# Kernel tuning notes

Hardware: AMD Instinct MI355X
Metric: run time of the kernel (lower is better)

## Reference

```python
import jax, jax.numpy as jnp
import numpy as np

B, TQ, TB, C, H, INNER = 4, 4096, 2048, 512, 8, 2048
D = C // H


def _ln(x, g, b, eps=1e-5):
    m = x.mean(-1, keepdims=True)
    v = ((x - m) ** 2).mean(-1, keepdims=True)
    return (x - m) / jnp.sqrt(v + eps) * g + b


def _heads(t):
    b, t_, _ = t.shape
    return t.reshape(b, t_, H, D).transpose(0, 2, 1, 3)  # (B,h,T,d)


def _merge(t):
    b, _, t_, _ = t.shape
    return t.transpose(0, 2, 1, 3).reshape(b, t_, C)


def _lin(x, w, b):
    return x @ w + b


def _forward(x, y0, y1,
             ln1_g, ln1_b, ln2_0_g, ln2_0_b, ln2_1_g, ln2_1_b,
             ln3_g, ln3_b, ln4_g, ln4_b, ln5_g, ln5_b,
             ca_q_w, ca_q_b, ca_k0_w, ca_k0_b, ca_v0_w, ca_v0_b,
             ca_k1_w, ca_k1_b, ca_v1_w, ca_v1_b, ca_p_w, ca_p_b,
             sa_q_w, sa_q_b, sa_k_w, sa_k_b, sa_v_w, sa_v_b, sa_p_w, sa_p_b,
             m1_w1, m1_b1, m1_w2, m1_b2, m2_w1, m2_b1, m2_w2, m2_b2):
    # ---- cross-attention (LinearCrossAttention, accumulate over branches) ----
    xn = _ln(x, ln1_g, ln1_b)
    q = jax.nn.softmax(_heads(_lin(xn, ca_q_w, ca_q_b)), axis=-1)  # (B,h,TQ,d)
    out = q
    branches = [(y0, ln2_0_g, ln2_0_b, ca_k0_w, ca_k0_b, ca_v0_w, ca_v0_b),
                (y1, ln2_1_g, ln2_1_b, ca_k1_w, ca_k1_b, ca_v1_w, ca_v1_b)]
    for yi, g, bb, kw, kb, vw, vb in branches:
        yn = _ln(yi, g, bb)
        k = jax.nn.softmax(_heads(_lin(yn, kw, kb)), axis=-1)  # (B,h,TB,d)
        v = _heads(_lin(yn, vw, vb))
        k_sum = k.sum(axis=-2, keepdims=True)                   # (B,h,1,d)
        d_inv = 1.0 / jnp.clip((q * k_sum).sum(-1, keepdims=True), 1e-9)
        ctx = jnp.einsum('bhtd,bhte->bhde', k, v)               # (B,h,d,d)
        out = out + (q @ ctx) * d_inv
    x = x + _lin(_merge(out), ca_p_w, ca_p_b)

    # ---- MLP 1 ----
    h1 = _lin(_ln(x, ln3_g, ln3_b), m1_w1, m1_b1)
    x = x + _lin(jax.nn.gelu(h1, approximate=False), m1_w2, m1_b2)

    # ---- self-attention (LinearAttention, attn_type='l1') ----
    xn = _ln(x, ln4_g, ln4_b)
    q = jax.nn.softmax(_heads(_lin(xn, sa_q_w, sa_q_b)), axis=-1)
    k = jax.nn.softmax(_heads(_lin(xn, sa_k_w, sa_k_b)), axis=-1)
    v = _heads(_lin(xn, sa_v_w, sa_v_b))
    k_sum = k.sum(axis=-2, keepdims=True)
    d_inv = 1.0 / (q * k_sum).sum(-1, keepdims=True)
    ctx = jnp.einsum('bhtd,bhte->bhde', k, v)
    sa = (q @ ctx) * d_inv + q
    x = x + _lin(_merge(sa), sa_p_w, sa_p_b)

    # ---- MLP 2 ----
    h2 = _lin(_ln(x, ln5_g, ln5_b), m2_w1, m2_b1)
    x = x + _lin(jax.nn.gelu(h2, approximate=False), m2_w2, m2_b2)
    return x


def setup_inputs() -> dict:
    key = jax.random.key(0)
    ks = iter(jax.random.split(key, 64))
    s = 1.0 / np.sqrt(C)
    si = 1.0 / np.sqrt(INNER)

    def lin_p(din, dout, scale):
        return (jax.random.normal(next(ks), (din, dout), jnp.float32) * scale,
                jnp.zeros((dout,), jnp.float32))

    inp = {
        'x': jax.random.normal(next(ks), (B, TQ, C), jnp.float32),
        'y0': jax.random.normal(next(ks), (B, TB, C), jnp.float32),
        'y1': jax.random.normal(next(ks), (B, TB, C), jnp.float32),
    }
    for nm in ['ln1', 'ln2_0', 'ln2_1', 'ln3', 'ln4', 'ln5']:
        inp[nm + '_g'] = jnp.ones((C,), jnp.float32)
        inp[nm + '_b'] = jnp.zeros((C,), jnp.float32)
    for nm in ['ca_q', 'ca_k0', 'ca_v0', 'ca_k1', 'ca_v1', 'ca_p',
               'sa_q', 'sa_k', 'sa_v', 'sa_p']:
        w, b = lin_p(C, C, s)
        inp[nm + '_w'] = w
        inp[nm + '_b'] = b
    for nm in ['m1', 'm2']:
        w1, b1 = lin_p(C, INNER, s)
        w2, b2 = lin_p(INNER, C, si)
        inp[nm + '_w1'], inp[nm + '_b1'] = w1, b1
        inp[nm + '_w2'], inp[nm + '_b2'] = w2, b2
    return inp


def reference(x, y0, y1,
              ln1_g, ln1_b, ln2_0_g, ln2_0_b, ln2_1_g, ln2_1_b,
              ln3_g, ln3_b, ln4_g, ln4_b, ln5_g, ln5_b,
              ca_q_w, ca_q_b, ca_k0_w, ca_k0_b, ca_v0_w, ca_v0_b,
              ca_k1_w, ca_k1_b, ca_v1_w, ca_v1_b, ca_p_w, ca_p_b,
              sa_q_w, sa_q_b, sa_k_w, sa_k_b, sa_v_w, sa_v_b, sa_p_w, sa_p_b,
              m1_w1, m1_b1, m1_w2, m1_b2, m2_w1, m2_b1, m2_w2, m2_b2):
    return _forward(x, y0, y1,
                    ln1_g, ln1_b, ln2_0_g, ln2_0_b, ln2_1_g, ln2_1_b,
                    ln3_g, ln3_b, ln4_g, ln4_b, ln5_g, ln5_b,
                    ca_q_w, ca_q_b, ca_k0_w, ca_k0_b, ca_v0_w, ca_v0_b,
                    ca_k1_w, ca_k1_b, ca_v1_w, ca_v1_b, ca_p_w, ca_p_b,
                    sa_q_w, sa_q_b, sa_k_w, sa_k_b, sa_v_w, sa_v_b, sa_p_w, sa_p_b,
                    m1_w1, m1_b1, m1_w2, m1_b2, m2_w1, m2_b1, m2_w2, m2_b2)
```

## Files before the change

### kernel.cpp

```cpp
#include <hip/hip_runtime.h>
#include <hip/hip_bf16.h>
#include <math.h>

#define NBATCH 4
#define TQD 4096
#define TBD 2048
#define CDIM 512
#define NH 8
#define HD 64
#define NINNER 2048

using short8 = __attribute__((ext_vector_type(8))) short;
using f32x4  = __attribute__((ext_vector_type(4))) float;

__device__ __forceinline__ float b2f(short s) {
  return __uint_as_float(((unsigned)(unsigned short)s) << 16);
}
__device__ __forceinline__ short f2b(float f) {
  unsigned u = __float_as_uint(f);
  return (short)((u + 0x7FFFu + ((u >> 16) & 1u)) >> 16);
}
__device__ __forceinline__ unsigned pk2(float a, float b) {
  float2 t; t.x = a; t.y = b;
  __hip_bfloat162 h = __float22bfloat162_rn(t);
  return *(unsigned*)&h;
}
__device__ __forceinline__ float gelu_fast(float x) {
  float x3 = x * x * x;
  float y2 = 1.5957691216f * (x + 0.044715f * x3);
  float e = __expf(y2);
  return x * e / (e + 1.0f);
}
__device__ __forceinline__ void gload16(const short* g, short* l) {
  __builtin_amdgcn_global_load_lds((const __attribute__((address_space(1))) void*)g,
                                   (__attribute__((address_space(3))) void*)l, 16, 0, 0);
}

__launch_bounds__(256)
__global__ void ln_kernel(const float* __restrict__ x, const float* __restrict__ g,
                          const float* __restrict__ b, short* __restrict__ out)
{
  int row = blockIdx.x * 4 + (threadIdx.x >> 6);
  int lane = threadIdx.x & 63;
  const float4* xp = (const float4*)(x + (size_t)row * CDIM);
  float4 v0 = xp[lane], v1 = xp[lane + 64];
  float s  = v0.x + v0.y + v0.z + v0.w + v1.x + v1.y + v1.z + v1.w;
  float s2 = v0.x * v0.x + v0.y * v0.y + v0.z * v0.z + v0.w * v0.w
           + v1.x * v1.x + v1.y * v1.y + v1.z * v1.z + v1.w * v1.w;
#pragma unroll
  for (int m = 1; m < 64; m <<= 1) { s += __shfl_xor(s, m); s2 += __shfl_xor(s2, m); }
  float mean = s * (1.0f / CDIM);
  float var  = s2 * (1.0f / CDIM) - mean * mean;
  float inv  = rsqrtf(var + 1e-5f);
  float4 g0 = ((const float4*)g)[lane], g1 = ((const float4*)g)[lane + 64];
  float4 b0 = ((const float4*)b)[lane], b1 = ((const float4*)b)[lane + 64];
  uint2 o0, o1;
  o0.x = pk2((v0.x - mean) * inv * g0.x + b0.x, (v0.y - mean) * inv * g0.y + b0.y);
  o0.y = pk2((v0.z - mean) * inv * g0.z + b0.z, (v0.w - mean) * inv * g0.w + b0.w);
  o1.x = pk2((v1.x - mean) * inv * g1.x + b1.x, (v1.y - mean) * inv * g1.y + b1.y);
  o1.y = pk2((v1.z - mean) * inv * g1.z + b1.z, (v1.w - mean) * inv * g1.w + b1.w);
  uint2* op = (uint2*)(out + (size_t)row * CDIM);
  op[lane] = o0;
  op[lane + 64] = o1;
}

struct TcvtDesc {
  const float* src[14];
  short* dst[14];
  int K[14], N[14], nblk[14];
};
__launch_bounds__(256)
__global__ void tcvt_all(TcvtDesc d)
{
  int blk = blockIdx.x, wi = 0;
  while (blk >= d.nblk[wi]) { blk -= d.nblk[wi]; wi++; }
  const float* __restrict__ W = d.src[wi];
  short* __restrict__ Wt = d.dst[wi];
  int K = d.K[wi], N = d.N[wi];
  __shared__ float t[32][33];
  int nbk = K >> 5;
  int bk = blk % nbk, bn = blk / nbk;
  int cx = threadIdx.x & 31, cy = threadIdx.x >> 5;
#pragma unroll
  for (int i = 0; i < 4; i++)
    t[cy + 8 * i][cx] = W[(size_t)(bk * 32 + cy + 8 * i) * N + bn * 32 + cx];
  __syncthreads();
#pragma unroll
  for (int i = 0; i < 4; i++)
    Wt[(size_t)(bn * 32 + cy + 8 * i) * K + bk * 32 + cx] = f2b(t[cx][cy + 8 * i]);
}

#define VMW(n) asm volatile("s_waitcnt vmcnt(" #n ")" ::: "memory");

template<int EPI>
__launch_bounds__(512, 4)
__global__ void gemm128(const short* __restrict__ A, const short* __restrict__ Bt,
                        const float* __restrict__ bias, const float* __restrict__ resid,
                        void* __restrict__ outp, int M, int N, int K, int smLimit,
                        float* __restrict__ ksumP, int csBase, int Trows)
{
  __shared__ short As[4 * 4096];
  __shared__ short Bs[2 * 8192];
  int tid = threadIdx.x, lane = tid & 63, wave = tid >> 6;
  int l15 = lane & 15, g = lane >> 4;
  int wr = wave >> 2, wn = wave & 3;
  int nbn = N >> 8;
  int per = gridDim.x >> 3;
  int wg = (blockIdx.x & 7) * per + (blockIdx.x >> 3);
  int bm = wg / nbn, bn = wg % nbn;
  f32x4 acc[4][4] = {};

  int srcslot = ((lane & 3) ^ ((lane >> 3) & 3)) * 8;
  const short* gA0 = A  + (size_t)(bm * 128 + wave * 16 + (lane >> 2)) * K + srcslot;
  const short* gB0 = Bt + (size_t)(bn * 256 + wave * 16 + (lane >> 2)) * K + srcslot;
  const short* gB1 = gB0 + (size_t)128 * K;
  short* lA = As + wave * 512;
  short* lB = Bs + wave * 512;

  int rsw = (g ^ ((l15 >> 1) & 3)) * 8;
  const short* raB = As + (wr * 64 + l15) * 32 + rsw;
  const short* rbB = Bs + (wn * 64 + l15) * 32 + rsw;

  short8 af[2], bfr[4];
  int NT = K >> 5;

#define STGA1(T) gload16(gA0 + (size_t)(T) * 32, lA + ((T) & 3) * 4096);
#define STGB1(T) { \
    gload16(gB0 + (size_t)(T) * 32, lB + ((T) & 1) * 8192); \
    gload16(gB1 + (size_t)(T) * 32, lB + ((T) & 1) * 8192 + 4096); }
#define RDB1(T) { \
    const short* bp = rbB + ((T) & 1) * 8192; \
    bfr[0] = *(const short8*)(bp);        bfr[1] = *(const short8*)(bp + 512); \
    bfr[2] = *(const short8*)(bp + 1024); bfr[3] = *(const short8*)(bp + 1536); }
#define RDA1(T, q) { \
    const short* ap = raB + ((T) & 3) * 4096 + (q) * 1024; \
    af[0] = *(const short8*)(ap); af[1] = *(const short8*)(ap + 512); }
#define MFMAQ1(q) { \
    __builtin_amdgcn_s_setprio(1); \
    _Pragma("unroll") for (int n = 0; n < 4; n++) { \
      acc[2*(q)][n]   = __builtin_amdgcn_mfma_f32_16x16x32_bf16(bfr[n], af[0], acc[2*(q)][n], 0, 0, 0); \
      acc[2*(q)+1][n] = __builtin_amdgcn_mfma_f32_16x16x32_bf16(bfr[n], af[1], acc[2*(q)+1][n], 0, 0, 0); } \
    __builtin_amdgcn_s_setprio(0); }
#define BARX1 { __builtin_amdgcn_s_barrier(); __builtin_amdgcn_sched_barrier(0); }
#define BAR21 { __builtin_amdgcn_s_barrier(); }

  STGB1(0); STGA1(0); STGA1(1);
  VMW(1);
  BAR21;

  for (int t = 0; t < NT - 2; ++t) {
    RDB1(t); RDA1(t, 0); STGB1(t + 1); BARX1; MFMAQ1(0); BAR21;
    RDA1(t, 1); STGA1(t + 2); VMW(1);  BARX1; MFMAQ1(1); BAR21;
  }
  {
    int t = NT - 2;
    RDB1(t); RDA1(t, 0); STGB1(t + 1); BARX1; MFMAQ1(0); BAR21;
    RDA1(t, 1); VMW(0);                BARX1; MFMAQ1(1); BAR21;
  }
  {
    int t = NT - 1;
    RDB1(t); RDA1(t, 0); BARX1; MFMAQ1(0); BAR21;
    RDA1(t, 1);          BARX1; MFMAQ1(1);
  }
#undef STGA1
#undef STGB1
#undef RDB1
#undef RDA1
#undef MFMAQ1
#undef BARX1
#undef BAR21

  int row0 = bm * 128 + wr * 64, col0 = bn * 256 + wn * 64;
#pragma unroll
  for (int n = 0; n < 4; n++) {
    f32x4 bz = *(const f32x4*)(bias + col0 + n * 16 + g * 4);
#pragma unroll
    for (int m = 0; m < 4; m++)
#pragma unroll
      for (int r = 0; r < 4; r++) acc[m][n][r] += bz[r];
  }
  if (EPI == 0 && col0 < smLimit) {
#pragma unroll
    for (int m = 0; m < 4; m++) {
      float mx = acc[m][0][0];
#pragma unroll
      for (int n = 0; n < 4; n++)
#pragma unroll
        for (int r = 0; r < 4; r++) mx = fmaxf(mx, acc[m][n][r]);
      mx = fmaxf(mx, __shfl_xor(mx, 16));
      mx = fmaxf(mx, __shfl_xor(mx, 32));
      float s = 0.0f;
#pragma unroll
      for (int n = 0; n < 4; n++)
#pragma unroll
        for (int r = 0; r < 4; r++) {
          float e = __expf(acc[m][n][r] - mx);
          acc[m][n][r] = e; s += e;
        }
      s += __shfl_xor(s, 16);
      s += __shfl_xor(s, 32);
      float inv = 1.0f / s;
#pragma unroll
      for (int n = 0; n < 4; n++)
#pragma unroll
        for (int r = 0; r < 4; r++) acc[m][n][r] *= inv;
    }
  }
  if (EPI == 0 && ksumP != nullptr) {
    unsigned rel = (unsigned)(col0 - csBase);
    if (rel < 512u) {
      float* kp = ksumP + ((row0 / Trows) * 8 + (int)(rel >> 6)) * 64;
#pragma unroll
      for (int n = 0; n < 4; n++) {
        f32x4 s = acc[0][n];
#pragma unroll
        for (int m = 1; m < 4; m++)
#pragma unroll
          for (int r = 0; r < 4; r++) s[r] += acc[m][n][r];
#pragma unroll
        for (int msk = 1; msk < 16; msk <<= 1)
#pragma unroll
          for (int r = 0; r < 4; r++) s[r] += __shfl_xor(s[r], msk);
        if (l15 == 0)
#pragma unroll
          for (int r = 0; r < 4; r++)
            atomicAdd(kp + n * 16 + g * 4 + r, s[r]);
      }
    }
  }
  if (EPI == 1) {
#pragma unroll
    for (int m = 0; m < 4; m++)
#pragma unroll
      for (int n = 0; n < 4; n++)
#pragma unroll
        for (int r = 0; r < 4; r++) acc[m][n][r] = gelu_fast(acc[m][n][r]);
  }
#pragma unroll
  for (int m = 0; m < 4; m++) {
    int row = row0 + m * 16 + l15;
#pragma unroll
    for (int n = 0; n < 4; n++) {
      size_t base = (size_t)row * N + col0 + n * 16 + g * 4;
      if (EPI == 2) {
        f32x4 rv = *(const f32x4*)(resid + base);
        f32x4 o;
#pragma unroll
        for (int r = 0; r < 4; r++) o[r] = rv[r] + acc[m][n][r];
        *(f32x4*)((float*)outp + base) = o;
      } else {
        uint2 u;
        u.x = pk2(acc[m][n][0], acc[m][n][1]);
        u.y = pk2(acc[m][n][2], acc[m][n][3]);
        *(uint2*)((unsigned short*)outp + base) = u;
      }
    }
  }
}

#define LDC 40
__launch_bounds__(256)
__global__ void ctx_kernel(const short* __restrict__ k, const short* __restrict__ v,
                           float* __restrict__ ctx, int T, int parts, int SD)
{
  __shared__ short kT[4][64 * LDC];
  __shared__ short vT[4][64 * LDC];
  int bh = blockIdx.x & 31, part = blockIdx.x >> 5;
  int b = bh >> 3, h = bh & 7;
  int tid = threadIdx.x, lane = tid & 63, wave = tid >> 6;
  int l15 = lane & 15, g = lane >> 4;
  int tlen = T / (4 * parts);
  int tbeg = (part * 4 + wave) * tlen;
  f32x4 acc[4][4] = {};
  short* myK = kT[wave];
  short* myV = vT[wave];
  for (int t0 = tbeg; t0 < tbeg + tlen; t0 += 32) {
#pragma unroll
    for (int j = 0; j < 4; j++) {
      int c = lane + j * 64;
      int r = c >> 3, d0 = (c & 7) * 8;
      short8 kv = *(const short8*)(k + (size_t)(b * T + t0 + r) * SD + h * 64 + d0);
      short8 vv = *(const short8*)(v + (size_t)(b * T + t0 + r) * SD + h * 64 + d0);
#pragma unroll
      for (int i = 0; i < 8; i++) {
        myK[(d0 + i) * LDC + r] = kv[i];
        myV[(d0 + i) * LDC + r] = vv[i];
      }
    }
    __syncthreads();
    short8 af[4], bfr[4];
#pragma unroll
    for (int m = 0; m < 4; m++) af[m]  = *(const short8*)(myK + (m * 16 + l15) * LDC + g * 8);
#pragma unroll
    for (int n = 0; n < 4; n++) bfr[n] = *(const short8*)(myV + (n * 16 + l15) * LDC + g * 8);
#pragma unroll
    for (int m = 0; m < 4; m++)
#pragma unroll
      for (int n = 0; n < 4; n++)
        acc[m][n] = __builtin_amdgcn_mfma_f32_16x16x32_bf16(af[m], bfr[n], acc[m][n], 0, 0, 0);
    __syncthreads();
  }
  float* cp = ctx + (size_t)bh * 64 * 64;
#pragma unroll
  for (int m = 0; m < 4; m++)
#pragma unroll
    for (int n = 0; n < 4; n++)
#pragma unroll
      for (int r = 0; r < 4; r++)
        atomicAdd(cp + (m * 16 + g * 4 + r) * 64 + (n * 16 + l15), acc[m][n][r]);
}

#define LQ 72
__launch_bounds__(256)
__global__ void qctx_kernel(const short* __restrict__ q,
                            const float* __restrict__ ctx,
                            const float* __restrict__ ksum,
                            short* __restrict__ outp, int T, int nb, int SD)
{
  __shared__ short qs[128 * LQ];
  __shared__ short cT[2][64 * LQ];
  __shared__ float dls[2][128];
  int ntb = T >> 7;
  int bh = blockIdx.x / ntb, tq = blockIdx.x % ntb;
  int b = bh >> 3, h = bh & 7;
  int tid = threadIdx.x, lane = tid & 63, wave = tid >> 6;
  int l15 = lane & 15, g = lane >> 4;
  size_t qbase = (size_t)(b * T + tq * 128) * SD + h * 64;
  size_t obase = (size_t)(b * T + tq * 128) * CDIM + h * 64;

#pragma unroll
  for (int j = 0; j < 4; j++) {
    int c = tid + j * 256;
    int r = c >> 3, d0 = (c & 7) * 8;
    *(short8*)(qs + r * LQ + d0) = *(const short8*)(q + qbase + (size_t)r * SD + d0);
  }
  for (int br = 0; br < nb; br++) {
    const float* cp = ctx + ((size_t)br * 32 + bh) * 4096;
#pragma unroll
    for (int j = 0; j < 16; j++) {
      int e2 = tid + j * 256;
      int dd = e2 >> 6, ee = e2 & 63;
      cT[br][ee * LQ + dd] = f2b(cp[e2]);
    }
  }
  __syncthreads();

  int r0 = wave * 32;
  for (int br = 0; br < nb; br++) {
    int row = r0 + (lane >> 1);
    int dbase = (lane & 1) * 32;
    const float* kp = ksum + ((size_t)br * 32 + bh) * 64 + dbase;
    float s = 0.0f;
#pragma unroll
    for (int d = 0; d < 32; d++)
      s += b2f(qs[row * LQ + dbase + d]) * kp[d];
    s += __shfl_xor(s, 1);
    if (!(lane & 1)) dls[br][row] = 1.0f / fmaxf(s, 1e-9f);
  }

  short8 af[2][2];
#pragma unroll
  for (int m = 0; m < 2; m++)
#pragma unroll
    for (int kk = 0; kk < 2; kk++)
      af[m][kk] = *(const short8*)(qs + (r0 + m * 16 + l15) * LQ + kk * 32 + g * 8);

  float ofin[2][4][4];
#pragma unroll
  for (int m = 0; m < 2; m++)
#pragma unroll
    for (int n = 0; n < 4; n++)
#pragma unroll
      for (int r = 0; r < 4; r++)
        ofin[m][n][r] = b2f(qs[(r0 + m * 16 + g * 4 + r) * LQ + n * 16 + l15]);

  for (int br = 0; br < nb; br++) {
    f32x4 acc[2][4] = {};
#pragma unroll
    for (int kk = 0; kk < 2; kk++) {
      short8 bfr[4];
#pragma unroll
      for (int n = 0; n < 4; n++)
        bfr[n] = *(const short8*)(cT[br] + (n * 16 + l15) * LQ + kk * 32 + g * 8);
#pragma unroll
      for (int m = 0; m < 2; m++)
#pragma unroll
        for (int n = 0; n < 4; n++)
          acc[m][n] = __builtin_amdgcn_mfma_f32_16x16x32_bf16(af[m][kk], bfr[n], acc[m][n], 0, 0, 0);
    }
#pragma unroll
    for (int m = 0; m < 2; m++)
#pragma unroll
      for (int n = 0; n < 4; n++)
#pragma unroll
        for (int r = 0; r < 4; r++)
          ofin[m][n][r] += dls[br][r0 + m * 16 + g * 4 + r] * acc[m][n][r];
  }

#pragma unroll
  for (int m = 0; m < 2; m++)
#pragma unroll
    for (int n = 0; n < 4; n++)
#pragma unroll
      for (int r = 0; r < 4; r++) {
        int row = r0 + m * 16 + g * 4 + r;
        int col = n * 16 + l15;
        outp[obase + (size_t)row * CDIM + col] = f2b(ofin[m][n][r]);
      }
}

extern "C" void kernel_launch(void* const* d_in, const int* in_sizes, int n_in,
                              void* d_out, int out_size, void* d_ws, size_t ws_size,
                              hipStream_t stream)
{
  (void)in_sizes; (void)n_in; (void)out_size; (void)ws_size;
  const float* x     = (const float*)d_in[0];
  const float* y0    = (const float*)d_in[1];
  const float* y1    = (const float*)d_in[2];
  const float* ln1g  = (const float*)d_in[3];
  const float* ln1b  = (const float*)d_in[4];
  const float* ln20g = (const float*)d_in[5];
  const float* ln20b = (const float*)d_in[6];
  const float* ln21g = (const float*)d_in[7];
  const float* ln21b = (const float*)d_in[8];
  const float* ln3g  = (const float*)d_in[9];
  const float* ln3b  = (const float*)d_in[10];
  const float* ln4g  = (const float*)d_in[11];
  const float* ln4b  = (const float*)d_in[12];
  const float* ln5g  = (const float*)d_in[13];
  const float* ln5b  = (const float*)d_in[14];
  const float* caqw  = (const float*)d_in[15];
  const float* caqb  = (const float*)d_in[16];
  const float* cak0w = (const float*)d_in[17];
  const float* cak0b = (const float*)d_in[18];
  const float* cav0w = (const float*)d_in[19];
  const float* cav0b = (const float*)d_in[20];
  const float* cak1w = (const float*)d_in[21];
  const float* cak1b = (const float*)d_in[22];
  const float* cav1w = (const float*)d_in[23];
  const float* cav1b = (const float*)d_in[24];
  const float* capw  = (const float*)d_in[25];
  const float* capb  = (const float*)d_in[26];
  const float* saqw  = (const float*)d_in[27];
  const float* saqb  = (const float*)d_in[28];
  const float* sakw  = (const float*)d_in[29];
  const float* sakb  = (const float*)d_in[30];
  const float* savw  = (const float*)d_in[31];
  const float* savb  = (const float*)d_in[32];
  const float* sapw  = (const float*)d_in[33];
  const float* sapb  = (const float*)d_in[34];
  const float* m1w1  = (const float*)d_in[35];
  const float* m1b1  = (const float*)d_in[36];
  const float* m1w2  = (const float*)d_in[37];
  const float* m1b2  = (const float*)d_in[38];
  const float* m2w1  = (const float*)d_in[39];
  const float* m2b1  = (const float*)d_in[40];
  const float* m2w2  = (const float*)d_in[41];
  const float* m2b2  = (const float*)d_in[42];
  float* xout = (float*)d_out;

  char* p = (char*)d_ws;
  size_t off = 0;
  auto take = [&](size_t bytes) {
    char* r = p + off;
    off += (bytes + 255) & ~(size_t)255;
    return r;
  };
  const size_t W512 = (size_t)512 * 512 * 2;
  const size_t WMLP = (size_t)2048 * 512 * 2;
  short* wt_caq   = (short*)take(W512);
  short* wt_cakv0 = (short*)take(2 * W512);
  short* wt_cakv1 = (short*)take(2 * W512);
  short* wt_cap   = (short*)take(W512);
  short* wt_saqkv = (short*)take(3 * W512);
  short* wt_sap   = (short*)take(W512);
  short* wt_m1w1  = (short*)take(WMLP);
  short* wt_m1w2  = (short*)take(WMLP);
  short* wt_m2w1  = (short*)take(WMLP);
  short* wt_m2w2  = (short*)take(WMLP);
  float* b_saqkv  = (float*)take(1536 * 4);
  float* b_cakv0  = (float*)take(1024 * 4);
  float* b_cakv1  = (float*)take(1024 * 4);
  short* xn   = (short*)take((size_t)16384 * 512 * 2);
  short* bufD = (short*)take((size_t)16384 * 512 * 2);
  short* big  = (short*)take((size_t)16384 * 1536 * 2);
  short* h1   = (short*)take((size_t)16384 * 2048 * 2);
  float* ksum = (float*)take((size_t)2 * 32 * 64 * 4);
  float* ctxb = (float*)take((size_t)2 * 32 * 64 * 64 * 4);

  short* q_ca  = big;
  short* kv_ca = big + (size_t)8 * 1024 * 1024;
  short* qkv   = big;

  const int MQ  = NBATCH * TQD;
  const int MKV = NBATCH * TBD;

  {
    TcvtDesc d;
    const float* srcs[14] = {caqw, cak0w, cav0w, cak1w, cav1w, capw,
                             saqw, sakw, savw, sapw, m1w1, m1w2, m2w1, m2w2};
    short* dsts[14] = {wt_caq, wt_cakv0, wt_cakv0 + 512 * 512,
                       wt_cakv1, wt_cakv1 + 512 * 512, wt_cap,
                       wt_saqkv, wt_saqkv + 512 * 512, wt_saqkv + 2 * 512 * 512, wt_sap,
                       wt_m1w1, wt_m1w2, wt_m2w1, wt_m2w2};
    int Ks[14] = {512,512,512,512,512,512,512,512,512,512, 512,2048,512,2048};
    int Ns[14] = {512,512,512,512,512,512,512,512,512,512, 2048,512,2048,512};
    int total = 0;
    for (int i = 0; i < 14; i++) {
      d.src[i] = srcs[i]; d.dst[i] = dsts[i]; d.K[i] = Ks[i]; d.N[i] = Ns[i];
      d.nblk[i] = (Ks[i] >> 5) * (Ns[i] >> 5);
      total += d.nblk[i];
    }
    tcvt_all<<<total, 256, 0, stream>>>(d);
  }
  hipMemcpyAsync(b_saqkv,        saqb,  512 * 4, hipMemcpyDeviceToDevice, stream);
  hipMemcpyAsync(b_saqkv + 512,  sakb,  512 * 4, hipMemcpyDeviceToDevice, stream);
  hipMemcpyAsync(b_saqkv + 1024, savb,  512 * 4, hipMemcpyDeviceToDevice, stream);
  hipMemcpyAsync(b_cakv0,        cak0b, 512 * 4, hipMemcpyDeviceToDevice, stream);
  hipMemcpyAsync(b_cakv0 + 512,  cav0b, 512 * 4, hipMemcpyDeviceToDevice, stream);
  hipMemcpyAsync(b_cakv1,        cak1b, 512 * 4, hipMemcpyDeviceToDevice, stream);
  hipMemcpyAsync(b_cakv1 + 512,  cav1b, 512 * 4, hipMemcpyDeviceToDevice, stream);

  ln_kernel<<<MQ / 4, 256, 0, stream>>>(x, ln1g, ln1b, xn);
  hipMemsetAsync(ksum, 0, (size_t)2 * 32 * 64 * 4, stream);
  hipMemsetAsync(ctxb, 0, (size_t)2 * 32 * 64 * 64 * 4, stream);
  gemm128<0><<<256, 512, 0, stream>>>(xn, wt_caq, caqb, nullptr, q_ca,
                                      MQ, 512, 512, 512, nullptr, 0, 0);
  for (int br = 0; br < 2; br++) {
    const float* yy = br ? y1 : y0;
    const float* lg = br ? ln21g : ln20g;
    const float* lb = br ? ln21b : ln20b;
    const short* wk = br ? wt_cakv1 : wt_cakv0;
    const float* bk = br ? b_cakv1 : b_cakv0;
    ln_kernel<<<MKV / 4, 256, 0, stream>>>(yy, lg, lb, bufD);
    gemm128<0><<<256, 512, 0, stream>>>(bufD, wk, bk, nullptr, kv_ca,
                                        MKV, 1024, 512, 512,
                                        ksum + (size_t)br * 2048, 0, TBD);
    ctx_kernel<<<256, 256, 0, stream>>>(kv_ca, kv_ca + 512,
                                        ctxb + (size_t)br * 32 * 4096, TBD, 8, 1024);
  }
  qctx_kernel<<<32 * (TQD / 128), 256, 0, stream>>>(q_ca, ctxb, ksum, bufD, TQD, 2, 512);
  gemm128<2><<<256, 512, 0, stream>>>(bufD, wt_cap, capb, x, xout,
                                      MQ, 512, 512, 0, nullptr, 0, 0);

  ln_kernel<<<MQ / 4, 256, 0, stream>>>(xout, ln3g, ln3b, xn);
  gemm128<1><<<1024, 512, 0, stream>>>(xn, wt_m1w1, m1b1, nullptr, h1,
                                       MQ, 2048, 512, 0, nullptr, 0, 0);
  gemm128<2><<<256, 512, 0, stream>>>(h1, wt_m1w2, m1b2, xout, xout,
                                      MQ, 512, 2048, 0, nullptr, 0, 0);

  ln_kernel<<<MQ / 4, 256, 0, stream>>>(xout, ln4g, ln4b, xn);
  hipMemsetAsync(ksum, 0, (size_t)32 * 64 * 4, stream);
  hipMemsetAsync(ctxb, 0, (size_t)32 * 64 * 64 * 4, stream);
  gemm128<0><<<768, 512, 0, stream>>>(xn, wt_saqkv, b_saqkv, nullptr, qkv,
                                      MQ, 1536, 512, 1024, ksum, 512, TQD);
  ctx_kernel<<<256, 256, 0, stream>>>(qkv + 512, qkv + 1024, ctxb, TQD, 8, 1536);
  qctx_kernel<<<32 * (TQD / 128), 256, 0, stream>>>(qkv, ctxb, ksum, bufD, TQD, 1, 1536);
  gemm128<2><<<256, 512, 0, stream>>>(bufD, wt_sap, sapb, xout, xout,
                                      MQ, 512, 512, 0, nullptr, 0, 0);

  ln_kernel<<<MQ / 4, 256, 0, stream>>>(xout, ln5g, ln5b, xn);
  gemm128<1><<<1024, 512, 0, stream>>>(xn, wt_m2w1, m2b1, nullptr, h1,
                                       MQ, 2048, 512, 0, nullptr, 0, 0);
  gemm128<2><<<256, 512, 0, stream>>>(h1, wt_m2w2, m2b2, xout, xout,
                                      MQ, 512, 2048, 0, nullptr, 0, 0);
}
```

Measured before the change: 563.7 us.

## Add narrow 128-column GEMM tile variant and triple-buffer B stage

Templates the GEMM on the N-tile width: a 128-column variant (NF=2) doubles the grid for the N=512 and N=1024 GEMMs, which previously ran only 256 blocks, to fill more CUs. The softmax epilogue for the narrow tile exchanges per-head row max and sum across paired waves through shared memory, because a 64-wide head now spans two waves. The B operand moves from double to triple buffering, with A and B prefetched two k-steps ahead. This costs more LDS and extra barriers in the softmax epilogue, and halves B-tile reuse per A load.

```diff
diff --git a/kernel.cpp b/kernel.cpp
--- a/kernel.cpp
+++ b/kernel.cpp
@@ -92,70 +92,73 @@
 
 #define VMW(n) asm volatile("s_waitcnt vmcnt(" #n ")" ::: "memory");
 
-template<int EPI>
+template<int EPI, int NF>
 __launch_bounds__(512, 4)
 __global__ void gemm128(const short* __restrict__ A, const short* __restrict__ Bt,
                         const float* __restrict__ bias, const float* __restrict__ resid,
                         void* __restrict__ outp, int M, int N, int K, int smLimit,
                         float* __restrict__ ksumP, int csBase, int Trows)
 {
+  constexpr int BUFB = NF * 2048;
   __shared__ short As[4 * 4096];
-  __shared__ short Bs[2 * 8192];
+  __shared__ short Bs[3 * BUFB];
   int tid = threadIdx.x, lane = tid & 63, wave = tid >> 6;
   int l15 = lane & 15, g = lane >> 4;
   int wr = wave >> 2, wn = wave & 3;
-  int nbn = N >> 8;
+  int nbn = N / (NF * 64);
   int per = gridDim.x >> 3;
   int wg = (blockIdx.x & 7) * per + (blockIdx.x >> 3);
   int bm = wg / nbn, bn = wg % nbn;
-  f32x4 acc[4][4] = {};
+  f32x4 acc[4][NF] = {};
 
   int srcslot = ((lane & 3) ^ ((lane >> 3) & 3)) * 8;
   const short* gA0 = A  + (size_t)(bm * 128 + wave * 16 + (lane >> 2)) * K + srcslot;
-  const short* gB0 = Bt + (size_t)(bn * 256 + wave * 16 + (lane >> 2)) * K + srcslot;
+  const short* gB0 = Bt + (size_t)(bn * (NF * 64) + wave * 16 + (lane >> 2)) * K + srcslot;
   const short* gB1 = gB0 + (size_t)128 * K;
   short* lA = As + wave * 512;
   short* lB = Bs + wave * 512;
 
   int rsw = (g ^ ((l15 >> 1) & 3)) * 8;
   const short* raB = As + (wr * 64 + l15) * 32 + rsw;
-  const short* rbB = Bs + (wn * 64 + l15) * 32 + rsw;
-
-  short8 af[2], bfr[4];
+  const short* rbB = Bs + (wn * (NF * 16) + l15) * 32 + rsw;
+
+  short8 af[2], bfr[NF];
   int NT = K >> 5;
 
 #define STGA1(T) gload16(gA0 + (size_t)(T) * 32, lA + ((T) & 3) * 4096);
 #define STGB1(T) { \
-    gload16(gB0 + (size_t)(T) * 32, lB + ((T) & 1) * 8192); \
-    gload16(gB1 + (size_t)(T) * 32, lB + ((T) & 1) * 8192 + 4096); }
+    gload16(gB0 + (size_t)(T) * 32, lB + ((T) % 3) * BUFB); \
+    if constexpr (NF == 4) gload16(gB1 + (size_t)(T) * 32, lB + ((T) % 3) * BUFB + 4096); }
 #define RDB1(T) { \
-    const short* bp = rbB + ((T) & 1) * 8192; \
-    bfr[0] = *(const short8*)(bp);        bfr[1] = *(const short8*)(bp + 512); \
-    bfr[2] = *(const short8*)(bp + 1024); bfr[3] = *(const short8*)(bp + 1536); }
+    const short* bp = rbB + ((T) % 3) * BUFB; \
+    _Pragma("unroll") for (int n = 0; n < NF; n++) \
+      bfr[n] = *(const short8*)(bp + n * 512); }
 #define RDA1(T, q) { \
     const short* ap = raB + ((T) & 3) * 4096 + (q) * 1024; \
     af[0] = *(const short8*)(ap); af[1] = *(const short8*)(ap + 512); }
 #define MFMAQ1(q) { \
     __builtin_amdgcn_s_setprio(1); \
-    _Pragma("unroll") for (int n = 0; n < 4; n++) { \
+    _Pragma("unroll") for (int n = 0; n < NF; n++) { \
       acc[2*(q)][n]   = __builtin_amdgcn_mfma_f32_16x16x32_bf16(bfr[n], af[0], acc[2*(q)][n], 0, 0, 0); \
       acc[2*(q)+1][n] = __builtin_amdgcn_mfma_f32_16x16x32_bf16(bfr[n], af[1], acc[2*(q)+1][n], 0, 0, 0); } \
     __builtin_amdgcn_s_setprio(0); }
+#define VMW_S { if constexpr (NF == 4) { VMW(3) } else { VMW(2) } }
 #define BARX1 { __builtin_amdgcn_s_barrier(); __builtin_amdgcn_sched_barrier(0); }
 #define BAR21 { __builtin_amdgcn_s_barrier(); }
 
-  STGB1(0); STGA1(0); STGA1(1);
-  VMW(1);
+  STGA1(0); STGB1(0);
+  STGA1(1); STGB1(1);
+  VMW_S;
   BAR21;
 
   for (int t = 0; t < NT - 2; ++t) {
-    RDB1(t); RDA1(t, 0); STGB1(t + 1); BARX1; MFMAQ1(0); BAR21;
-    RDA1(t, 1); STGA1(t + 2); VMW(1);  BARX1; MFMAQ1(1); BAR21;
+    RDB1(t); RDA1(t, 0); STGA1(t + 2); STGB1(t + 2); BARX1; MFMAQ1(0); BAR21;
+    RDA1(t, 1); VMW_S;                               BARX1; MFMAQ1(1); BAR21;
   }
   {
     int t = NT - 2;
-    RDB1(t); RDA1(t, 0); STGB1(t + 1); BARX1; MFMAQ1(0); BAR21;
-    RDA1(t, 1); VMW(0);                BARX1; MFMAQ1(1); BAR21;
+    RDB1(t); RDA1(t, 0); BARX1; MFMAQ1(0); BAR21;
+    RDA1(t, 1); VMW(0);  BARX1; MFMAQ1(1); BAR21;
   }
   {
     int t = NT - 1;
@@ -167,51 +170,108 @@
 #undef RDB1
 #undef RDA1
 #undef MFMAQ1
+#undef VMW_S
 #undef BARX1
 #undef BAR21
 
-  int row0 = bm * 128 + wr * 64, col0 = bn * 256 + wn * 64;
-#pragma unroll
-  for (int n = 0; n < 4; n++) {
+  int row0 = bm * 128 + wr * 64, col0 = bn * (NF * 64) + wn * (NF * 16);
+#pragma unroll
+  for (int n = 0; n < NF; n++) {
     f32x4 bz = *(const f32x4*)(bias + col0 + n * 16 + g * 4);
 #pragma unroll
     for (int m = 0; m < 4; m++)
 #pragma unroll
       for (int r = 0; r < 4; r++) acc[m][n][r] += bz[r];
   }
-  if (EPI == 0 && col0 < smLimit) {
-#pragma unroll
-    for (int m = 0; m < 4; m++) {
-      float mx = acc[m][0][0];
-#pragma unroll
-      for (int n = 0; n < 4; n++)
-#pragma unroll
-        for (int r = 0; r < 4; r++) mx = fmaxf(mx, acc[m][n][r]);
-      mx = fmaxf(mx, __shfl_xor(mx, 16));
-      mx = fmaxf(mx, __shfl_xor(mx, 32));
-      float s = 0.0f;
-#pragma unroll
-      for (int n = 0; n < 4; n++)
-#pragma unroll
-        for (int r = 0; r < 4; r++) {
-          float e = __expf(acc[m][n][r] - mx);
-          acc[m][n][r] = e; s += e;
+  if (EPI == 0) {
+    bool insm = (bn * (NF * 64) < smLimit);
+    if constexpr (NF == 4) {
+      if (insm) {
+#pragma unroll
+        for (int m = 0; m < 4; m++) {
+          float mx = acc[m][0][0];
+#pragma unroll
+          for (int n = 0; n < 4; n++)
+#pragma unroll
+            for (int r = 0; r < 4; r++) mx = fmaxf(mx, acc[m][n][r]);
+          mx = fmaxf(mx, __shfl_xor(mx, 16));
+          mx = fmaxf(mx, __shfl_xor(mx, 32));
+          float s = 0.0f;
+#pragma unroll
+          for (int n = 0; n < 4; n++)
+#pragma unroll
+            for (int r = 0; r < 4; r++) {
+              float e = __expf(acc[m][n][r] - mx);
+              acc[m][n][r] = e; s += e;
+            }
+          s += __shfl_xor(s, 16);
+          s += __shfl_xor(s, 32);
+          float inv = 1.0f / s;
+#pragma unroll
+          for (int n = 0; n < 4; n++)
+#pragma unroll
+            for (int r = 0; r < 4; r++) acc[m][n][r] *= inv;
         }
-      s += __shfl_xor(s, 16);
-      s += __shfl_xor(s, 32);
-      float inv = 1.0f / s;
-#pragma unroll
-      for (int n = 0; n < 4; n++)
-#pragma unroll
-        for (int r = 0; r < 4; r++) acc[m][n][r] *= inv;
+      }
+    } else {
+      if (insm) {
+        float* xch = (float*)As;
+        float pm[4], ps[4];
+#pragma unroll
+        for (int m = 0; m < 4; m++) {
+          float mx = acc[m][0][0];
+#pragma unroll
+          for (int n = 0; n < 2; n++)
+#pragma unroll
+            for (int r = 0; r < 4; r++) mx = fmaxf(mx, acc[m][n][r]);
+          mx = fmaxf(mx, __shfl_xor(mx, 16));
+          mx = fmaxf(mx, __shfl_xor(mx, 32));
+          pm[m] = mx;
+        }
+        __syncthreads();
+        if (g == 0)
+#pragma unroll
+          for (int m = 0; m < 4; m++) xch[wave * 64 + m * 16 + l15] = pm[m];
+        __syncthreads();
+#pragma unroll
+        for (int m = 0; m < 4; m++)
+          pm[m] = fmaxf(pm[m], xch[(wave ^ 1) * 64 + m * 16 + l15]);
+#pragma unroll
+        for (int m = 0; m < 4; m++) {
+          float s = 0.0f;
+#pragma unroll
+          for (int n = 0; n < 2; n++)
+#pragma unroll
+            for (int r = 0; r < 4; r++) {
+              float e = __expf(acc[m][n][r] - pm[m]);
+              acc[m][n][r] = e; s += e;
+            }
+          s += __shfl_xor(s, 16);
+          s += __shfl_xor(s, 32);
+          ps[m] = s;
+        }
+        __syncthreads();
+        if (g == 0)
+#pragma unroll
+          for (int m = 0; m < 4; m++) xch[wave * 64 + m * 16 + l15] = ps[m];
+        __syncthreads();
+#pragma unroll
+        for (int m = 0; m < 4; m++) {
+          float inv = 1.0f / (ps[m] + xch[(wave ^ 1) * 64 + m * 16 + l15]);
+#pragma unroll
+          for (int n = 0; n < 2; n++)
+#pragma unroll
+            for (int r = 0; r < 4; r++) acc[m][n][r] *= inv;
+        }
+      }
     }
   }
   if (EPI == 0 && ksumP != nullptr) {
     unsigned rel = (unsigned)(col0 - csBase);
     if (rel < 512u) {
-      float* kp = ksumP + ((row0 / Trows) * 8 + (int)(rel >> 6)) * 64;
-#pragma unroll
-      for (int n = 0; n < 4; n++) {
+      float* kp = ksumP + ((row0 / Trows) * 8 + (int)(rel >> 6)) * 64 + (int)(rel & 63u);
+#pragma unroll
+      for (int n = 0; n < NF; n++) {
         f32x4 s = acc[0][n];
 #pragma unroll
         for (int m = 1; m < 4; m++)
@@ -232,7 +292,7 @@
 #pragma unroll
     for (int m = 0; m < 4; m++)
 #pragma unroll
-      for (int n = 0; n < 4; n++)
+      for (int n = 0; n < NF; n++)
 #pragma unroll
         for (int r = 0; r < 4; r++) acc[m][n][r] = gelu_fast(acc[m][n][r]);
   }
@@ -240,7 +300,7 @@
   for (int m = 0; m < 4; m++) {
     int row = row0 + m * 16 + l15;
 #pragma unroll
-    for (int n = 0; n < 4; n++) {
+    for (int n = 0; n < NF; n++) {
       size_t base = (size_t)row * N + col0 + n * 16 + g * 4;
       if (EPI == 2) {
         f32x4 rv = *(const f32x4*)(resid + base);
@@ -524,8 +584,8 @@
   ln_kernel<<<MQ / 4, 256, 0, stream>>>(x, ln1g, ln1b, xn);
   hipMemsetAsync(ksum, 0, (size_t)2 * 32 * 64 * 4, stream);
   hipMemsetAsync(ctxb, 0, (size_t)2 * 32 * 64 * 64 * 4, stream);
-  gemm128<0><<<256, 512, 0, stream>>>(xn, wt_caq, caqb, nullptr, q_ca,
-                                      MQ, 512, 512, 512, nullptr, 0, 0);
+  gemm128<0, 2><<<512, 512, 0, stream>>>(xn, wt_caq, caqb, nullptr, q_ca,
+                                         MQ, 512, 512, 512, nullptr, 0, 0);
   for (int br = 0; br < 2; br++) {
     const float* yy = br ? y1 : y0;
     const float* lg = br ? ln21g : ln20g;
@@ -533,35 +593,35 @@
     const short* wk = br ? wt_cakv1 : wt_cakv0;
     const float* bk = br ? b_cakv1 : b_cakv0;
     ln_kernel<<<MKV / 4, 256, 0, stream>>>(yy, lg, lb, bufD);
-    gemm128<0><<<256, 512, 0, stream>>>(bufD, wk, bk, nullptr, kv_ca,
-                                        MKV, 1024, 512, 512,
-                                        ksum + (size_t)br * 2048, 0, TBD);
+    gemm128<0, 2><<<512, 512, 0, stream>>>(bufD, wk, bk, nullptr, kv_ca,
+                                           MKV, 1024, 512, 512,
+                                           ksum + (size_t)br * 2048, 0, TBD);
     ctx_kernel<<<256, 256, 0, stream>>>(kv_ca, kv_ca + 512,
                                         ctxb + (size_t)br * 32 * 4096, TBD, 8, 1024);
   }
   qctx_kernel<<<32 * (TQD / 128), 256, 0, stream>>>(q_ca, ctxb, ksum, bufD, TQD, 2, 512);
-  gemm128<2><<<256, 512, 0, stream>>>(bufD, wt_cap, capb, x, xout,
-                                      MQ, 512, 512, 0, nullptr, 0, 0);
+  gemm128<2, 2><<<512, 512, 0, stream>>>(bufD, wt_cap, capb, x, xout,
+                                         MQ, 512, 512, 0, nullptr, 0, 0);
 
   ln_kernel<<<MQ / 4, 256, 0, stream>>>(xout, ln3g, ln3b, xn);
-  gemm128<1><<<1024, 512, 0, stream>>>(xn, wt_m1w1, m1b1, nullptr, h1,
-                                       MQ, 2048, 512, 0, nullptr, 0, 0);
-  gemm128<2><<<256, 512, 0, stream>>>(h1, wt_m1w2, m1b2, xout, xout,
-                                      MQ, 512, 2048, 0, nullptr, 0, 0);
+  gemm128<1, 4><<<1024, 512, 0, stream>>>(xn, wt_m1w1, m1b1, nullptr, h1,
+                                          MQ, 2048, 512, 0, nullptr, 0, 0);
+  gemm128<2, 2><<<512, 512, 0, stream>>>(h1, wt_m1w2, m1b2, xout, xout,
+                                         MQ, 512, 2048, 0, nullptr, 0, 0);
 
   ln_kernel<<<MQ / 4, 256, 0, stream>>>(xout, ln4g, ln4b, xn);
   hipMemsetAsync(ksum, 0, (size_t)32 * 64 * 4, stream);
   hipMemsetAsync(ctxb, 0, (size_t)32 * 64 * 64 * 4, stream);
-  gemm128<0><<<768, 512, 0, stream>>>(xn, wt_saqkv, b_saqkv, nullptr, qkv,
-                                      MQ, 1536, 512, 1024, ksum, 512, TQD);
+  gemm128<0, 4><<<768, 512, 0, stream>>>(xn, wt_saqkv, b_saqkv, nullptr, qkv,
+                                         MQ, 1536, 512, 1024, ksum, 512, TQD);
   ctx_kernel<<<256, 256, 0, stream>>>(qkv + 512, qkv + 1024, ctxb, TQD, 8, 1536);
   qctx_kernel<<<32 * (TQD / 128), 256, 0, stream>>>(qkv, ctxb, ksum, bufD, TQD, 1, 1536);
-  gemm128<2><<<256, 512, 0, stream>>>(bufD, wt_sap, sapb, xout, xout,
-                                      MQ, 512, 512, 0, nullptr, 0, 0);
+  gemm128<2, 2><<<512, 512, 0, stream>>>(bufD, wt_sap, sapb, xout, xout,
+                                         MQ, 512, 512, 0, nullptr, 0, 0);
 
   ln_kernel<<<MQ / 4, 256, 0, stream>>>(xout, ln5g, ln5b, xn);
-  gemm128<1><<<1024, 512, 0, stream>>>(xn, wt_m2w1, m2b1, nullptr, h1,
-                                       MQ, 2048, 512, 0, nullptr, 0, 0);
-  gemm128<2><<<256, 512, 0, stream>>>(h1, wt_m2w2, m2b2, xout, xout,
-                                      MQ, 512, 2048, 0, nullptr, 0, 0);
-}
+  gemm128<1, 4><<<1024, 512, 0, stream>>>(xn, wt_m2w1, m2b1, nullptr, h1,
+                                          MQ, 2048, 512, 0, nullptr, 0, 0);
+  gemm128<2, 2><<<512, 512, 0, stream>>>(h1, wt_m2w2, m2b2, xout, xout,
+                                         MQ, 512, 2048, 0, nullptr, 0, 0);
+}
```

Result: no change. 559.1 us (-0.8%).

## Pre-pack GEMM operands into MFMA fragment layout and load directly to registers

Applied to the files above, without the earlier changes.

Producers (layernorm, weight conversion, GELU epilogue, qctx output) now write bf16 operands in a fragment-packed layout (paOff), so each wave can load MFMA fragments straight from global memory into registers. This replaces the LDS-staged, barrier-synchronised GEMM with an LDS-free 128x128 tile kernel with register double buffering. It removes LDS traffic and barriers at the cost of more redundant global/L2 reads per tile and smaller tiles.

```diff
diff --git a/kernel.cpp b/kernel.cpp
--- a/kernel.cpp
+++ b/kernel.cpp
@@ -31,9 +31,9 @@
   float e = __expf(y2);
   return x * e / (e + 1.0f);
 }
-__device__ __forceinline__ void gload16(const short* g, short* l) {
-  __builtin_amdgcn_global_load_lds((const __attribute__((address_space(1))) void*)g,
-                                   (__attribute__((address_space(3))) void*)l, 16, 0, 0);
+__device__ __forceinline__ size_t paOff(int r, int k, int NKG) {
+  return ((size_t)((r >> 4) * NKG + (k >> 5)) * 64 + (r & 15) + 16 * ((k >> 3) & 3)) * 8
+         + (k & 7);
 }
 
 __launch_bounds__(256)
@@ -43,7 +43,7 @@
   int row = blockIdx.x * 4 + (threadIdx.x >> 6);
   int lane = threadIdx.x & 63;
   const float4* xp = (const float4*)(x + (size_t)row * CDIM);
-  float4 v0 = xp[lane], v1 = xp[lane + 64];
+  float4 v0 = xp[2 * lane], v1 = xp[2 * lane + 1];
   float s  = v0.x + v0.y + v0.z + v0.w + v1.x + v1.y + v1.z + v1.w;
   float s2 = v0.x * v0.x + v0.y * v0.y + v0.z * v0.z + v0.w * v0.w
            + v1.x * v1.x + v1.y * v1.y + v1.z * v1.z + v1.w * v1.w;
@@ -52,16 +52,14 @@
   float mean = s * (1.0f / CDIM);
   float var  = s2 * (1.0f / CDIM) - mean * mean;
   float inv  = rsqrtf(var + 1e-5f);
-  float4 g0 = ((const float4*)g)[lane], g1 = ((const float4*)g)[lane + 64];
-  float4 b0 = ((const float4*)b)[lane], b1 = ((const float4*)b)[lane + 64];
-  uint2 o0, o1;
-  o0.x = pk2((v0.x - mean) * inv * g0.x + b0.x, (v0.y - mean) * inv * g0.y + b0.y);
-  o0.y = pk2((v0.z - mean) * inv * g0.z + b0.z, (v0.w - mean) * inv * g0.w + b0.w);
-  o1.x = pk2((v1.x - mean) * inv * g1.x + b1.x, (v1.y - mean) * inv * g1.y + b1.y);
-  o1.y = pk2((v1.z - mean) * inv * g1.z + b1.z, (v1.w - mean) * inv * g1.w + b1.w);
-  uint2* op = (uint2*)(out + (size_t)row * CDIM);
-  op[lane] = o0;
-  op[lane + 64] = o1;
+  float4 g0 = ((const float4*)g)[2 * lane], g1 = ((const float4*)g)[2 * lane + 1];
+  float4 b0 = ((const float4*)b)[2 * lane], b1 = ((const float4*)b)[2 * lane + 1];
+  uint4 o;
+  o.x = pk2((v0.x - mean) * inv * g0.x + b0.x, (v0.y - mean) * inv * g0.y + b0.y);
+  o.y = pk2((v0.z - mean) * inv * g0.z + b0.z, (v0.w - mean) * inv * g0.w + b0.w);
+  o.z = pk2((v1.x - mean) * inv * g1.x + b1.x, (v1.y - mean) * inv * g1.y + b1.y);
+  o.w = pk2((v1.z - mean) * inv * g1.z + b1.z, (v1.w - mean) * inv * g1.w + b1.w);
+  *(uint4*)(out + paOff(row, 8 * lane, CDIM >> 5)) = o;
 }
 
 struct TcvtDesc {
@@ -86,91 +84,56 @@
     t[cy + 8 * i][cx] = W[(size_t)(bk * 32 + cy + 8 * i) * N + bn * 32 + cx];
   __syncthreads();
 #pragma unroll
-  for (int i = 0; i < 4; i++)
-    Wt[(size_t)(bn * 32 + cy + 8 * i) * K + bk * 32 + cx] = f2b(t[cx][cy + 8 * i]);
-}
-
-#define VMW(n) asm volatile("s_waitcnt vmcnt(" #n ")" ::: "memory");
-
-template<int EPI>
-__launch_bounds__(512, 4)
-__global__ void gemm128(const short* __restrict__ A, const short* __restrict__ Bt,
-                        const float* __restrict__ bias, const float* __restrict__ resid,
-                        void* __restrict__ outp, int M, int N, int K, int smLimit,
-                        float* __restrict__ ksumP, int csBase, int Trows)
+  for (int i = 0; i < 4; i++) {
+    int n = bn * 32 + cy + 8 * i, k = bk * 32 + cx;
+    Wt[paOff(n, k, K >> 5)] = f2b(t[cx][cy + 8 * i]);
+  }
+}
+
+template<int EPI, int KK>
+__launch_bounds__(256, 3)
+__global__ void gemmd(const short* __restrict__ A, const short* __restrict__ Bt,
+                      const float* __restrict__ bias, const float* __restrict__ resid,
+                      void* __restrict__ outp, int M, int N, int smLimit,
+                      float* __restrict__ ksumP, int csBase, int Trows)
 {
-  __shared__ short As[4 * 4096];
-  __shared__ short Bs[2 * 8192];
+  constexpr int NKG = KK >> 5;
+  constexpr int NT = NKG;
   int tid = threadIdx.x, lane = tid & 63, wave = tid >> 6;
   int l15 = lane & 15, g = lane >> 4;
-  int wr = wave >> 2, wn = wave & 3;
-  int nbn = N >> 8;
+  int wr = wave >> 1, wn = wave & 1;
+  int nbn = N >> 7;
   int per = gridDim.x >> 3;
   int wg = (blockIdx.x & 7) * per + (blockIdx.x >> 3);
   int bm = wg / nbn, bn = wg % nbn;
   f32x4 acc[4][4] = {};
 
-  int srcslot = ((lane & 3) ^ ((lane >> 3) & 3)) * 8;
-  const short* gA0 = A  + (size_t)(bm * 128 + wave * 16 + (lane >> 2)) * K + srcslot;
-  const short* gB0 = Bt + (size_t)(bn * 256 + wave * 16 + (lane >> 2)) * K + srcslot;
-  const short* gB1 = gB0 + (size_t)128 * K;
-  short* lA = As + wave * 512;
-  short* lB = Bs + wave * 512;
-
-  int rsw = (g ^ ((l15 >> 1) & 3)) * 8;
-  const short* raB = As + (wr * 64 + l15) * 32 + rsw;
-  const short* rbB = Bs + (wn * 64 + l15) * 32 + rsw;
-
-  short8 af[2], bfr[4];
-  int NT = K >> 5;
-
-#define STGA1(T) gload16(gA0 + (size_t)(T) * 32, lA + ((T) & 3) * 4096);
-#define STGB1(T) { \
-    gload16(gB0 + (size_t)(T) * 32, lB + ((T) & 1) * 8192); \
-    gload16(gB1 + (size_t)(T) * 32, lB + ((T) & 1) * 8192 + 4096); }
-#define RDB1(T) { \
-    const short* bp = rbB + ((T) & 1) * 8192; \
-    bfr[0] = *(const short8*)(bp);        bfr[1] = *(const short8*)(bp + 512); \
-    bfr[2] = *(const short8*)(bp + 1024); bfr[3] = *(const short8*)(bp + 1536); }
-#define RDA1(T, q) { \
-    const short* ap = raB + ((T) & 3) * 4096 + (q) * 1024; \
-    af[0] = *(const short8*)(ap); af[1] = *(const short8*)(ap + 512); }
-#define MFMAQ1(q) { \
+  const short* pa = A  + (size_t)(bm * 8 + wr * 4) * NKG * 512 + lane * 8;
+  const short* pb = Bt + (size_t)(bn * 8 + wn * 4) * NKG * 512 + lane * 8;
+
+  short8 X[8], Y[8];
+#define LDF(kg, Z) { \
+    _Pragma("unroll") for (int f = 0; f < 4; f++) { \
+      Z[f]     = *(const short8*)(pa + ((size_t)f * NKG + (kg)) * 512); \
+      Z[4 + f] = *(const short8*)(pb + ((size_t)f * NKG + (kg)) * 512); } }
+#define CMP(Z) { \
     __builtin_amdgcn_s_setprio(1); \
-    _Pragma("unroll") for (int n = 0; n < 4; n++) { \
-      acc[2*(q)][n]   = __builtin_amdgcn_mfma_f32_16x16x32_bf16(bfr[n], af[0], acc[2*(q)][n], 0, 0, 0); \
-      acc[2*(q)+1][n] = __builtin_amdgcn_mfma_f32_16x16x32_bf16(bfr[n], af[1], acc[2*(q)+1][n], 0, 0, 0); } \
+    _Pragma("unroll") for (int mq = 0; mq < 4; mq++) \
+      _Pragma("unroll") for (int nq = 0; nq < 4; nq++) \
+        acc[mq][nq] = __builtin_amdgcn_mfma_f32_16x16x32_bf16(Z[4 + nq], Z[mq], acc[mq][nq], 0, 0, 0); \
     __builtin_amdgcn_s_setprio(0); }
-#define BARX1 { __builtin_amdgcn_s_barrier(); __builtin_amdgcn_sched_barrier(0); }
-#define BAR21 { __builtin_amdgcn_s_barrier(); }
-
-  STGB1(0); STGA1(0); STGA1(1);
-  VMW(1);
-  BAR21;
-
-  for (int t = 0; t < NT - 2; ++t) {
-    RDB1(t); RDA1(t, 0); STGB1(t + 1); BARX1; MFMAQ1(0); BAR21;
-    RDA1(t, 1); STGA1(t + 2); VMW(1);  BARX1; MFMAQ1(1); BAR21;
-  }
-  {
-    int t = NT - 2;
-    RDB1(t); RDA1(t, 0); STGB1(t + 1); BARX1; MFMAQ1(0); BAR21;
-    RDA1(t, 1); VMW(0);                BARX1; MFMAQ1(1); BAR21;
-  }
-  {
-    int t = NT - 1;
-    RDB1(t); RDA1(t, 0); BARX1; MFMAQ1(0); BAR21;
-    RDA1(t, 1);          BARX1; MFMAQ1(1);
-  }
-#undef STGA1
-#undef STGB1
-#undef RDB1
-#undef RDA1
-#undef MFMAQ1
-#undef BARX1
-#undef BAR21
-
-  int row0 = bm * 128 + wr * 64, col0 = bn * 256 + wn * 64;
+
+  LDF(0, X); LDF(1, Y);
+#pragma unroll 2
+  for (int t = 0; t < NT - 2; t += 2) {
+    CMP(X); LDF(t + 2, X);
+    CMP(Y); LDF(t + 3, Y);
+  }
+  CMP(X); CMP(Y);
+#undef LDF
+#undef CMP
+
+  int row0 = bm * 128 + wr * 64, col0 = bn * 128 + wn * 64;
 #pragma unroll
   for (int n = 0; n < 4; n++) {
     f32x4 bz = *(const f32x4*)(bias + col0 + n * 16 + g * 4);
@@ -228,27 +191,26 @@
       }
     }
   }
-  if (EPI == 1) {
-#pragma unroll
-    for (int m = 0; m < 4; m++)
-#pragma unroll
-      for (int n = 0; n < 4; n++)
-#pragma unroll
-        for (int r = 0; r < 4; r++) acc[m][n][r] = gelu_fast(acc[m][n][r]);
-  }
 #pragma unroll
   for (int m = 0; m < 4; m++) {
     int row = row0 + m * 16 + l15;
 #pragma unroll
     for (int n = 0; n < 4; n++) {
-      size_t base = (size_t)row * N + col0 + n * 16 + g * 4;
       if (EPI == 2) {
+        size_t base = (size_t)row * N + col0 + n * 16 + g * 4;
         f32x4 rv = *(const f32x4*)(resid + base);
         f32x4 o;
 #pragma unroll
         for (int r = 0; r < 4; r++) o[r] = rv[r] + acc[m][n][r];
         *(f32x4*)((float*)outp + base) = o;
+      } else if (EPI == 1) {
+        int k0 = col0 + n * 16 + g * 4;
+        uint2 u;
+        u.x = pk2(gelu_fast(acc[m][n][0]), gelu_fast(acc[m][n][1]));
+        u.y = pk2(gelu_fast(acc[m][n][2]), gelu_fast(acc[m][n][3]));
+        *(uint2*)((short*)outp + paOff(row, k0, N >> 5)) = u;
       } else {
+        size_t base = (size_t)row * N + col0 + n * 16 + g * 4;
         uint2 u;
         u.x = pk2(acc[m][n][0], acc[m][n][1]);
         u.y = pk2(acc[m][n][2], acc[m][n][3]);
@@ -326,7 +288,7 @@
   int tid = threadIdx.x, lane = tid & 63, wave = tid >> 6;
   int l15 = lane & 15, g = lane >> 4;
   size_t qbase = (size_t)(b * T + tq * 128) * SD + h * 64;
-  size_t obase = (size_t)(b * T + tq * 128) * CDIM + h * 64;
+  int grow0 = b * T + tq * 128;
 
 #pragma unroll
   for (int j = 0; j < 4; j++) {
@@ -404,8 +366,8 @@
 #pragma unroll
       for (int r = 0; r < 4; r++) {
         int row = r0 + m * 16 + g * 4 + r;
-        int col = n * 16 + l15;
-        outp[obase + (size_t)row * CDIM + col] = f2b(ofin[m][n][r]);
+        int kcol = h * 64 + n * 16 + l15;
+        outp[paOff(grow0 + row, kcol, CDIM >> 5)] = f2b(ofin[m][n][r]);
       }
 }
 
@@ -524,8 +486,8 @@
   ln_kernel<<<MQ / 4, 256, 0, stream>>>(x, ln1g, ln1b, xn);
   hipMemsetAsync(ksum, 0, (size_t)2 * 32 * 64 * 4, stream);
   hipMemsetAsync(ctxb, 0, (size_t)2 * 32 * 64 * 64 * 4, stream);
-  gemm128<0><<<256, 512, 0, stream>>>(xn, wt_caq, caqb, nullptr, q_ca,
-                                      MQ, 512, 512, 512, nullptr, 0, 0);
+  gemmd<0, 512><<<512, 256, 0, stream>>>(xn, wt_caq, caqb, nullptr, q_ca,
+                                         MQ, 512, 512, nullptr, 0, 0);
   for (int br = 0; br < 2; br++) {
     const float* yy = br ? y1 : y0;
     const float* lg = br ? ln21g : ln20g;
@@ -533,35 +495,35 @@
     const short* wk = br ? wt_cakv1 : wt_cakv0;
     const float* bk = br ? b_cakv1 : b_cakv0;
     ln_kernel<<<MKV / 4, 256, 0, stream>>>(yy, lg, lb, bufD);
-    gemm128<0><<<256, 512, 0, stream>>>(bufD, wk, bk, nullptr, kv_ca,
-                                        MKV, 1024, 512, 512,
-                                        ksum + (size_t)br * 2048, 0, TBD);
+    gemmd<0, 512><<<512, 256, 0, stream>>>(bufD, wk, bk, nullptr, kv_ca,
+                                           MKV, 1024, 512,
+                                           ksum + (size_t)br * 2048, 0, TBD);
     ctx_kernel<<<256, 256, 0, stream>>>(kv_ca, kv_ca + 512,
                                         ctxb + (size_t)br * 32 * 4096, TBD, 8, 1024);
   }
   qctx_kernel<<<32 * (TQD / 128), 256, 0, stream>>>(q_ca, ctxb, ksum, bufD, TQD, 2, 512);
-  gemm128<2><<<256, 512, 0, stream>>>(bufD, wt_cap, capb, x, xout,
-                                      MQ, 512, 512, 0, nullptr, 0, 0);
+  gemmd<2, 512><<<512, 256, 0, stream>>>(bufD, wt_cap, capb, x, xout,
+                                         MQ, 512, 0, nullptr, 0, 0);
 
   ln_kernel<<<MQ / 4, 256, 0, stream>>>(xout, ln3g, ln3b, xn);
-  gemm128<1><<<1024, 512, 0, stream>>>(xn, wt_m1w1, m1b1, nullptr, h1,
-                                       MQ, 2048, 512, 0, nullptr, 0, 0);
-  gemm128<2><<<256, 512, 0, stream>>>(h1, wt_m1w2, m1b2, xout, xout,
-                                      MQ, 512, 2048, 0, nullptr, 0, 0);
+  gemmd<1, 512><<<2048, 256, 0, stream>>>(xn, wt_m1w1, m1b1, nullptr, h1,
+                                          MQ, 2048, 0, nullptr, 0, 0);
+  gemmd<2, 2048><<<512, 256, 0, stream>>>(h1, wt_m1w2, m1b2, xout, xout,
+                                          MQ, 512, 0, nullptr, 0, 0);
 
   ln_kernel<<<MQ / 4, 256, 0, stream>>>(xout, ln4g, ln4b, xn);
   hipMemsetAsync(ksum, 0, (size_t)32 * 64 * 4, stream);
   hipMemsetAsync(ctxb, 0, (size_t)32 * 64 * 64 * 4, stream);
-  gemm128<0><<<768, 512, 0, stream>>>(xn, wt_saqkv, b_saqkv, nullptr, qkv,
-                                      MQ, 1536, 512, 1024, ksum, 512, TQD);
+  gemmd<0, 512><<<1536, 256, 0, stream>>>(xn, wt_saqkv, b_saqkv, nullptr, qkv,
+                                          MQ, 1536, 1024, ksum, 512, TQD);
   ctx_kernel<<<256, 256, 0, stream>>>(qkv + 512, qkv + 1024, ctxb, TQD, 8, 1536);
   qctx_kernel<<<32 * (TQD / 128), 256, 0, stream>>>(qkv, ctxb, ksum, bufD, TQD, 1, 1536);
-  gemm128<2><<<256, 512, 0, stream>>>(bufD, wt_sap, sapb, xout, xout,
-                                      MQ, 512, 512, 0, nullptr, 0, 0);
+  gemmd<2, 512><<<512, 256, 0, stream>>>(bufD, wt_sap, sapb, xout, xout,
+                                         MQ, 512, 0, nullptr, 0, 0);
 
   ln_kernel<<<MQ / 4, 256, 0, stream>>>(xout, ln5g, ln5b, xn);
-  gemm128<1><<<1024, 512, 0, stream>>>(xn, wt_m2w1, m2b1, nullptr, h1,
-                                       MQ, 2048, 512, 0, nullptr, 0, 0);
-  gemm128<2><<<256, 512, 0, stream>>>(h1, wt_m2w2, m2b2, xout, xout,
-                                      MQ, 512, 2048, 0, nullptr, 0, 0);
-}
+  gemmd<1, 512><<<2048, 256, 0, stream>>>(xn, wt_m2w1, m2b1, nullptr, h1,
+                                          MQ, 2048, 0, nullptr, 0, 0);
+  gemmd<2, 2048><<<512, 256, 0, stream>>>(h1, wt_m2w2, m2b2, xout, xout,
+                                          MQ, 512, 0, nullptr, 0, 0);
+}
```

Measured after the change: 540.9 us (median of 2 runs). 4.0% less time.
